# Kernel tuning notes

Hardware: AMD Instinct MI355X
Metric: run time of the kernel (lower is better)

The kernel has to match this reference:

```python
import jax, jax.numpy as jnp
import numpy as np

D_IN = 2048
D_OUT = 2048
NUM_HEADS = 16
NUM_GROUPS = 4
HEAD_DIM = D_OUT // NUM_HEADS          # 128
HEADS_PER_GROUP = NUM_HEADS // NUM_GROUPS  # 4


def setup_inputs() -> dict:
    key = jax.random.key(0)
    ks = jax.random.split(key, 6)
    b, s = 2, 2048
    x = jax.random.normal(ks[0], (b, s, D_IN), dtype=jnp.float32)
    # Store weights as [in, out] so y = x @ W (equivalent to torch Linear x @ W.T)
    sc_q = 1.0 / np.sqrt(D_IN)
    Wq = jax.random.uniform(ks[1], (D_IN, D_OUT), jnp.float32, -sc_q, sc_q)
    Wk = jax.random.uniform(ks[2], (D_IN, NUM_GROUPS * HEAD_DIM), jnp.float32, -sc_q, sc_q)
    Wv = jax.random.uniform(ks[3], (D_IN, NUM_GROUPS * HEAD_DIM), jnp.float32, -sc_q, sc_q)
    sc_o = 1.0 / np.sqrt(D_OUT)
    Wo = jax.random.uniform(ks[4], (D_OUT, D_OUT), jnp.float32, -sc_o, sc_o)
    bo = jax.random.uniform(ks[5], (D_OUT,), jnp.float32, -sc_o, sc_o)
    return {"x": x, "Wq": Wq, "Wk": Wk, "Wv": Wv, "Wo": Wo, "bo": bo}


def reference(x, Wq, Wk, Wv, Wo, bo):
    b, s, _ = x.shape
    g, hpg, hd = NUM_GROUPS, HEADS_PER_GROUP, HEAD_DIM
    # Projections; keep grouped layout instead of repeat_interleave (same math)
    q = (x @ Wq).reshape(b, s, g, hpg, hd)   # query heads ordered group-major,
                                             # matching repeat_interleave of K/V
    k = (x @ Wk).reshape(b, s, g, hd)
    v = (x @ Wv).reshape(b, s, g, hd)
    # scores: [b, g, hpg, q_len, k_len]
    scores = jnp.einsum('bqghd,bkgd->bghqk', q, k)
    causal = jnp.triu(jnp.ones((s, s), dtype=bool), k=1)  # True above diagonal
    scores = jnp.where(causal, -jnp.inf, scores)
    scale = 1.0 / jnp.sqrt(jnp.asarray(hd, dtype=scores.dtype))
    attn = jax.nn.softmax(scores * scale, axis=-1)
    ctx = jnp.einsum('bghqk,bkgd->bqghd', attn, v).reshape(b, s, D_OUT)
    return ctx @ Wo + bo
```

## Files before the change

### kernel.cpp

```cpp
#include <hip/hip_runtime.h>

typedef short v8s __attribute__((ext_vector_type(8)));
typedef float v4f __attribute__((ext_vector_type(4)));

__device__ __forceinline__ short f2bf(float f) {
  union { float f; unsigned u; } v; v.f = f;
  unsigned r = v.u + 0x7FFFu + ((v.u >> 16) & 1u);
  return (short)(r >> 16);
}

__device__ __forceinline__ void gll16(const short* g, short* l) {
  __builtin_amdgcn_global_load_lds(
      (const __attribute__((address_space(1))) void*)g,
      (__attribute__((address_space(3))) void*)l, 16, 0, 0);
}

__global__ void cast_f32_bf16(const float* __restrict__ in, short* __restrict__ out, int n4) {
  int i = blockIdx.x * blockDim.x + threadIdx.x;
  if (i >= n4) return;
  float4 v = ((const float4*)in)[i];
  short4 o;
  o.x = f2bf(v.x); o.y = f2bf(v.y); o.z = f2bf(v.z); o.w = f2bf(v.w);
  ((short4*)out)[i] = o;
}

__global__ void cast_transpose_weights(const float* __restrict__ Wq, const float* __restrict__ Wk,
                                       const float* __restrict__ Wv, const float* __restrict__ Wo,
                                       short* __restrict__ Wqkvt, short* __restrict__ Wot) {
  __shared__ float tile[32][33];
  const int tx = threadIdx.x, ty = threadIdx.y;
  int bx = blockIdx.x;
  const float* src; short* dst; int C, cb;
  if (bx < 64)      { src = Wq; dst = Wqkvt;                        C = 2048; cb = bx; }
  else if (bx < 80) { src = Wk; dst = Wqkvt + (size_t)2048 * 2048;  C = 512;  cb = bx - 64; }
  else if (bx < 96) { src = Wv; dst = Wqkvt + (size_t)2560 * 2048;  C = 512;  cb = bx - 80; }
  else              { src = Wo; dst = Wot;                          C = 2048; cb = bx - 96; }
  const int c0 = cb * 32, r0 = blockIdx.y * 32;
#pragma unroll
  for (int i = 0; i < 4; ++i)
    tile[ty + 8 * i][tx] = src[(size_t)(r0 + ty + 8 * i) * C + c0 + tx];
  __syncthreads();
#pragma unroll
  for (int i = 0; i < 4; ++i)
    dst[(size_t)(c0 + ty + 8 * i) * 2048 + r0 + tx] = f2bf(tile[tx][ty + 8 * i]);
}

__global__ void transpose_v_perm(const short* __restrict__ qkv, short* __restrict__ out) {
  __shared__ short tile[32][33];
  const int tx = threadIdx.x, ty = threadIdx.y;
  const int c0 = blockIdx.x * 32, r0 = blockIdx.y * 32;
  const int z = blockIdx.z;
#pragma unroll
  for (int i = 0; i < 4; ++i)
    tile[ty + 8 * i][tx] = qkv[(size_t)(z * 2048 + r0 + ty + 8 * i) * 3072 + 2560 + c0 + tx];
  __syncthreads();
#pragma unroll
  for (int i = 0; i < 4; ++i) {
    int k = r0 + tx;
    int pk = (k & ~31) | ((((k >> 2) & 3) * 2 + ((k >> 4) & 1)) * 4) | (k & 3);
    out[(size_t)z * 512 * 2048 + (size_t)(c0 + ty + 8 * i) * 2048 + pk] = tile[tx][ty + 8 * i];
  }
}

template <int BF16_OUT>
__global__ __launch_bounds__(256) void gemm_bt(const short* __restrict__ A,
                                               const short* __restrict__ Bt,
                                               void* __restrict__ Cout,
                                               const float* __restrict__ bias,
                                               int M, int N, int K) {
  __shared__ short As[128 * 32];
  __shared__ short Bs[128 * 32];
  const int tid = threadIdx.x;
  const int m0 = blockIdx.y * 128, n0 = blockIdx.x * 128;
  const int w = tid >> 6, lane = tid & 63, quad = lane >> 4, l16 = lane & 15;
  const int wm = (w >> 1) * 64, wn = (w & 1) * 64;
  v4f acc[4][4] = {};
  const int srow = lane >> 2, scol = (lane & 3) * 8;
  const short* Ap = A + (size_t)(m0 + w * 32 + srow) * K + scol;
  const short* Bp = Bt + (size_t)(n0 + w * 32 + srow) * K + scol;
  short* AsW = &As[(w * 32) * 32 + lane * 8];
  short* BsW = &Bs[(w * 32) * 32 + lane * 8];
  const size_t rstep = (size_t)16 * K;
  for (int k0 = 0; k0 < K; k0 += 32) {
    __syncthreads();
    gll16(Ap, AsW);
    gll16(Ap + rstep, AsW + 16 * 32);
    gll16(Bp, BsW);
    gll16(Bp + rstep, BsW + 16 * 32);
    __syncthreads();
    Ap += 32; Bp += 32;
    v8s af[4], bf[4];
#pragma unroll
    for (int i = 0; i < 4; ++i) af[i] = *(const v8s*)&As[(wm + i * 16 + l16) * 32 + quad * 8];
#pragma unroll
    for (int i = 0; i < 4; ++i) bf[i] = *(const v8s*)&Bs[(wn + i * 16 + l16) * 32 + quad * 8];
#pragma unroll
    for (int mi = 0; mi < 4; ++mi)
#pragma unroll
      for (int ni = 0; ni < 4; ++ni)
        acc[mi][ni] = __builtin_amdgcn_mfma_f32_16x16x32_bf16(af[mi], bf[ni], acc[mi][ni], 0, 0, 0);
  }
#pragma unroll
  for (int mi = 0; mi < 4; ++mi) {
#pragma unroll
    for (int ni = 0; ni < 4; ++ni) {
      const int col = n0 + wn + ni * 16 + l16;
#pragma unroll
      for (int r = 0; r < 4; ++r) {
        const int row = m0 + wm + mi * 16 + quad * 4 + r;
        if (BF16_OUT) {
          ((short*)Cout)[(size_t)row * N + col] = f2bf(acc[mi][ni][r]);
        } else {
          ((float*)Cout)[(size_t)row * N + col] = acc[mi][ni][r] + bias[col];
        }
      }
    }
  }
}

__global__ __launch_bounds__(256, 1) void flash_attn4(const short* __restrict__ QKV,
                                                      const short* __restrict__ Vtb,
                                                      short* __restrict__ ctx) {
  __shared__ __align__(16) short smem[32768];
  const int tid = threadIdx.x;
  const int w = tid >> 6, lane = tid & 63, quad = lane >> 4, l16 = lane & 15;
  const int wq = w >> 1, wk = w & 1;
  const int bh = blockIdx.y;
  const int b = bh >> 4, h = bh & 15, g = h >> 2;
  const float scale = 0.08838834764831845f;
  v8s ones;
#pragma unroll
  for (int i = 0; i < 8; ++i) ones[i] = (short)0x3F80;

  const int krl = lane >> 4, kcl = lane & 15;
  const int vrl = lane >> 3, vcl = lane & 7;
  const short* Kg0 = QKV + (size_t)(b * 2048 + w * 16 + krl) * 3072 + 2048 + g * 128;
  const short* Vg0 = Vtb + (size_t)(b * 512 + g * 128 + w * 32 + vrl) * 2048 + (vcl ^ (vrl & 7)) * 8;
  short* kd = smem + (w * 16) * 128 + lane * 8;
  short* vd = smem + 8192 + (w * 32) * 64 + lane * 8;

  auto stage = [&](int key0, int bs) {
    const short* kg = Kg0 + (size_t)key0 * 3072;
    const short* vg = Vg0 + key0;
#pragma unroll
    for (int ii = 0; ii < 4; ++ii) {
      const int rl = (ii * 4 + krl) & 15;
      gll16(kg + (size_t)(ii * 4) * 3072 + (kcl ^ rl) * 8, kd + bs * 16384 + ii * 512);
      gll16(vg + (size_t)(ii * 8) * 2048, vd + bs * 16384 + ii * 512);
    }
  };

  float* red = (float*)smem;

#pragma unroll 1
  for (int half = 0; half < 2; ++half) {
    const int qt = half ? (15 - blockIdx.x) : blockIdx.x;
    const int q0 = qt * 128;
    const int qb = q0 + wq * 64;

    v8s aq[4][4];
#pragma unroll
    for (int qs = 0; qs < 4; ++qs) {
      const short* Qp = QKV + (size_t)(b * 2048 + qb + qs * 16 + l16) * 3072 + h * 128 + quad * 8;
#pragma unroll
      for (int kk = 0; kk < 4; ++kk) aq[qs][kk] = *(const v8s*)(Qp + kk * 32);
    }
    v4f o[4][8] = {};
    v4f ol[4] = {};

    __syncthreads();
    stage(0, 0);
    const int nk = 2 * qt + 2;
#pragma unroll 1
    for (int kt = 0; kt < nk; ++kt) {
      const int key0 = kt << 6;
      __syncthreads();
      if (kt + 1 < nk) stage((kt + 1) << 6, (kt + 1) & 1);
      const short* Ks = smem + (kt & 1) * 16384;
      const short* Vs = Ks + 8192;
      const int kb = key0 + wk * 32;
      if (kb > qb + 63) continue;
      v4f sf[4][2] = {};
#pragma unroll
      for (int kfl = 0; kfl < 2; ++kfl)
#pragma unroll
        for (int kk = 0; kk < 4; ++kk) {
          v8s kfr = *(const v8s*)&Ks[((wk * 2 + kfl) * 16 + l16) * 128 + (((kk * 4 + quad) ^ l16) * 8)];
#pragma unroll
          for (int qs = 0; qs < 4; ++qs)
            sf[qs][kfl] = __builtin_amdgcn_mfma_f32_16x16x32_bf16(kfr, aq[qs][kk], sf[qs][kfl], 0, 0, 0);
        }
      const bool diag = (kb + 31 > qb);
      v8s pa[4];
#pragma unroll
      for (int qs = 0; qs < 4; ++qs) {
        const int qg = qb + qs * 16 + l16;
        v8s t;
#pragma unroll
        for (int kfl = 0; kfl < 2; ++kfl)
#pragma unroll
          for (int r = 0; r < 4; ++r) {
            float s = sf[qs][kfl][r] * scale;
            if (diag && (kb + kfl * 16 + quad * 4 + r > qg)) s = -1e30f;
            t[kfl * 4 + r] = f2bf(__expf(s));
          }
        pa[qs] = t;
      }
#pragma unroll
      for (int nf = 0; nf < 8; ++nf) {
        v8s vf = *(const v8s*)&Vs[(nf * 16 + l16) * 64 + (((wk * 4 + quad) ^ (l16 & 7)) * 8)];
#pragma unroll
        for (int qs = 0; qs < 4; ++qs)
          o[qs][nf] = __builtin_amdgcn_mfma_f32_16x16x32_bf16(pa[qs], vf, o[qs][nf], 0, 0, 0);
      }
#pragma unroll
      for (int qs = 0; qs < 4; ++qs)
        ol[qs] = __builtin_amdgcn_mfma_f32_16x16x32_bf16(pa[qs], ones, ol[qs], 0, 0, 0);
    }
    __syncthreads();

    if (wk == 1) {
#pragma unroll
      for (int qs = 0; qs < 4; ++qs)
        *(v4f*)&red[(wq * 4 + qs) * 256 + l16 * 16 + quad * 4] = ol[qs];
    }
    __syncthreads();
    if (wk == 0) {
#pragma unroll
      for (int qs = 0; qs < 4; ++qs)
        ol[qs] += *(const v4f*)&red[(wq * 4 + qs) * 256 + l16 * 16 + quad * 4];
    }
    __syncthreads();
    if (wk == 1) {
#pragma unroll
      for (int qs = 0; qs < 4; ++qs)
#pragma unroll
        for (int nf = 0; nf < 8; ++nf)
          *(v4f*)&red[(((wq * 4 + qs) * 8 + nf) * 256) + l16 * 16 + quad * 4] = o[qs][nf];
    }
    __syncthreads();
    if (wk == 0) {
#pragma unroll
      for (int qs = 0; qs < 4; ++qs) {
        float inv[4];
#pragma unroll
        for (int r = 0; r < 4; ++r) inv[r] = 1.0f / ol[qs][r];
#pragma unroll
        for (int nf = 0; nf < 8; ++nf) {
          v4f osum = o[qs][nf] + *(const v4f*)&red[(((wq * 4 + qs) * 8 + nf) * 256) + l16 * 16 + quad * 4];
#pragma unroll
          for (int r = 0; r < 4; ++r) {
            const int row = qb + qs * 16 + quad * 4 + r;
            ctx[(size_t)(b * 2048 + row) * 2048 + h * 128 + nf * 16 + l16] = f2bf(osum[r] * inv[r]);
          }
        }
      }
    }
  }
}

extern "C" void kernel_launch(void* const* d_in, const int* in_sizes, int n_in,
                              void* d_out, int out_size, void* d_ws, size_t ws_size,
                              hipStream_t stream) {
  const float* x = (const float*)d_in[0];
  const float* Wq = (const float*)d_in[1];
  const float* Wk = (const float*)d_in[2];
  const float* Wv = (const float*)d_in[3];
  const float* Wo = (const float*)d_in[4];
  const float* bo = (const float*)d_in[5];
  float* out = (float*)d_out;
  char* ws = (char*)d_ws;

  short* xb    = (short*)(ws);
  short* ctx   = (short*)(ws);
  short* Wqkvt = (short*)(ws + 16777216);
  short* Wot   = (short*)(ws + 29360128);
  short* QKV   = (short*)(ws + 37748736);
  short* Vtb   = (short*)(ws + 62914560);

  dim3 tb(32, 8);
  cast_f32_bf16<<<8192, 256, 0, stream>>>(x, xb, 2097152);
  cast_transpose_weights<<<dim3(160, 64), tb, 0, stream>>>(Wq, Wk, Wv, Wo, Wqkvt, Wot);

  gemm_bt<1><<<dim3(24, 32), 256, 0, stream>>>(xb, Wqkvt, (void*)QKV, nullptr, 4096, 3072, 2048);

  transpose_v_perm<<<dim3(16, 64, 2), tb, 0, stream>>>(QKV, Vtb);

  flash_attn4<<<dim3(8, 32), 256, 0, stream>>>(QKV, Vtb, ctx);

  gemm_bt<0><<<dim3(16, 32), 256, 0, stream>>>(ctx, Wot, (void*)out, bo, 4096, 2048, 2048);
}
```

Before: 335.0 us.

## Split attention keys across four waves and fold softmax scale into Q projection

The attention kernel moves to 512 threads with four key-split waves per query half, processing 128-key tiles from a single-buffered LDS stage instead of double-buffered 64-key tiles. The softmax scale and log2(e) are folded into the Q projection epilogue so the inner loop uses exp2f without a multiply. Partial sums from the four key waves are reduced through LDS in several sequential steps. The aim is more parallelism and fewer ALU ops per score, at the cost of losing load/compute overlap and adding reduction barriers.

```diff
diff --git a/kernel.cpp b/kernel.cpp
--- a/kernel.cpp
+++ b/kernel.cpp
@@ -62,12 +62,12 @@
   }
 }
 
-template <int BF16_OUT>
+template <int BF16_OUT, int SCALEQ>
 __global__ __launch_bounds__(256) void gemm_bt(const short* __restrict__ A,
                                                const short* __restrict__ Bt,
                                                void* __restrict__ Cout,
                                                const float* __restrict__ bias,
-                                               int M, int N, int K) {
+                                               int M, int N, int K, float qalpha) {
   __shared__ short As[128 * 32];
   __shared__ short Bs[128 * 32];
   const int tid = threadIdx.x;
@@ -105,11 +105,12 @@
 #pragma unroll
     for (int ni = 0; ni < 4; ++ni) {
       const int col = n0 + wn + ni * 16 + l16;
+      const float cs = (SCALEQ && col < 2048) ? qalpha : 1.0f;
 #pragma unroll
       for (int r = 0; r < 4; ++r) {
         const int row = m0 + wm + mi * 16 + quad * 4 + r;
         if (BF16_OUT) {
-          ((short*)Cout)[(size_t)row * N + col] = f2bf(acc[mi][ni][r]);
+          ((short*)Cout)[(size_t)row * N + col] = f2bf(acc[mi][ni][r] * cs);
         } else {
           ((float*)Cout)[(size_t)row * N + col] = acc[mi][ni][r] + bias[col];
         }
@@ -118,37 +119,27 @@
   }
 }
 
-__global__ __launch_bounds__(256, 1) void flash_attn4(const short* __restrict__ QKV,
+__global__ __launch_bounds__(512, 2) void flash_attn5(const short* __restrict__ QKV,
                                                       const short* __restrict__ Vtb,
                                                       short* __restrict__ ctx) {
   __shared__ __align__(16) short smem[32768];
+  short* Ks = smem;
+  short* Vs = smem + 16384;
   const int tid = threadIdx.x;
   const int w = tid >> 6, lane = tid & 63, quad = lane >> 4, l16 = lane & 15;
-  const int wq = w >> 1, wk = w & 1;
+  const int wq = w >> 2, wk = w & 3;
   const int bh = blockIdx.y;
   const int b = bh >> 4, h = bh & 15, g = h >> 2;
-  const float scale = 0.08838834764831845f;
   v8s ones;
 #pragma unroll
   for (int i = 0; i < 8; ++i) ones[i] = (short)0x3F80;
 
-  const int krl = lane >> 4, kcl = lane & 15;
-  const int vrl = lane >> 3, vcl = lane & 7;
-  const short* Kg0 = QKV + (size_t)(b * 2048 + w * 16 + krl) * 3072 + 2048 + g * 128;
-  const short* Vg0 = Vtb + (size_t)(b * 512 + g * 128 + w * 32 + vrl) * 2048 + (vcl ^ (vrl & 7)) * 8;
-  short* kd = smem + (w * 16) * 128 + lane * 8;
-  short* vd = smem + 8192 + (w * 32) * 64 + lane * 8;
-
-  auto stage = [&](int key0, int bs) {
-    const short* kg = Kg0 + (size_t)key0 * 3072;
-    const short* vg = Vg0 + key0;
-#pragma unroll
-    for (int ii = 0; ii < 4; ++ii) {
-      const int rl = (ii * 4 + krl) & 15;
-      gll16(kg + (size_t)(ii * 4) * 3072 + (kcl ^ rl) * 8, kd + bs * 16384 + ii * 512);
-      gll16(vg + (size_t)(ii * 8) * 2048, vd + bs * 16384 + ii * 512);
-    }
-  };
+  const int srow0 = w * 16 + (lane >> 4);
+  const int slot = lane & 15;
+  short* kdst = Ks + srow0 * 128 + slot * 8;
+  short* vdst = Vs + srow0 * 128 + slot * 8;
+  const short* Kg0 = QKV + (size_t)(b * 2048 + srow0) * 3072 + 2048 + g * 128;
+  const short* Vg0 = Vtb + (size_t)(b * 512 + g * 128 + srow0) * 2048;
 
   float* red = (float*)smem;
 
@@ -168,24 +159,30 @@
     v4f o[4][8] = {};
     v4f ol[4] = {};
 
-    __syncthreads();
-    stage(0, 0);
-    const int nk = 2 * qt + 2;
+    const int nk = qt + 1;
 #pragma unroll 1
     for (int kt = 0; kt < nk; ++kt) {
-      const int key0 = kt << 6;
+      const int key0 = kt << 7;
       __syncthreads();
-      if (kt + 1 < nk) stage((kt + 1) << 6, (kt + 1) & 1);
-      const short* Ks = smem + (kt & 1) * 16384;
-      const short* Vs = Ks + 8192;
+      {
+#pragma unroll
+        for (int ii = 0; ii < 4; ++ii) {
+          const int rlow = (lane >> 4) + ii * 4;
+          gll16(Kg0 + (size_t)(key0 + ii * 4) * 3072 + (slot ^ rlow) * 8, kdst + ii * 4 * 128);
+          gll16(Vg0 + (size_t)(ii * 4) * 2048 + key0 + (slot ^ rlow) * 8, vdst + ii * 4 * 128);
+        }
+      }
+      __syncthreads();
+
       const int kb = key0 + wk * 32;
       if (kb > qb + 63) continue;
+
       v4f sf[4][2] = {};
 #pragma unroll
       for (int kfl = 0; kfl < 2; ++kfl)
 #pragma unroll
         for (int kk = 0; kk < 4; ++kk) {
-          v8s kfr = *(const v8s*)&Ks[((wk * 2 + kfl) * 16 + l16) * 128 + (((kk * 4 + quad) ^ l16) * 8)];
+          v8s kfr = *(const v8s*)&Ks[(wk * 32 + kfl * 16 + l16) * 128 + (((kk * 4 + quad) ^ l16) * 8)];
 #pragma unroll
           for (int qs = 0; qs < 4; ++qs)
             sf[qs][kfl] = __builtin_amdgcn_mfma_f32_16x16x32_bf16(kfr, aq[qs][kk], sf[qs][kfl], 0, 0, 0);
@@ -200,15 +197,15 @@
         for (int kfl = 0; kfl < 2; ++kfl)
 #pragma unroll
           for (int r = 0; r < 4; ++r) {
-            float s = sf[qs][kfl][r] * scale;
+            float s = sf[qs][kfl][r];
             if (diag && (kb + kfl * 16 + quad * 4 + r > qg)) s = -1e30f;
-            t[kfl * 4 + r] = f2bf(__expf(s));
+            t[kfl * 4 + r] = f2bf(exp2f(s));
           }
         pa[qs] = t;
       }
 #pragma unroll
       for (int nf = 0; nf < 8; ++nf) {
-        v8s vf = *(const v8s*)&Vs[(nf * 16 + l16) * 64 + (((wk * 4 + quad) ^ (l16 & 7)) * 8)];
+        v8s vf = *(const v8s*)&Vs[(nf * 16 + l16) * 128 + (((wk * 4 + quad) ^ l16) * 8)];
 #pragma unroll
         for (int qs = 0; qs < 4; ++qs)
           o[qs][nf] = __builtin_amdgcn_mfma_f32_16x16x32_bf16(pa[qs], vf, o[qs][nf], 0, 0, 0);
@@ -217,44 +214,67 @@
       for (int qs = 0; qs < 4; ++qs)
         ol[qs] = __builtin_amdgcn_mfma_f32_16x16x32_bf16(pa[qs], ones, ol[qs], 0, 0, 0);
     }
-    __syncthreads();
-
+
+    __syncthreads();
+#pragma unroll
+    for (int qs = 0; qs < 4; ++qs)
+      *(v4f*)&red[(((wk * 2 + wq) * 4 + qs) * 256) + l16 * 16 + quad * 4] = ol[qs];
+    __syncthreads();
+    float inv[4][4];
+    if (wk == 0) {
+#pragma unroll
+      for (int qs = 0; qs < 4; ++qs) {
+        v4f lsum = ol[qs];
+#pragma unroll
+        for (int j = 1; j < 4; ++j)
+          lsum += *(const v4f*)&red[(((j * 2 + wq) * 4 + qs) * 256) + l16 * 16 + quad * 4];
+#pragma unroll
+        for (int r = 0; r < 4; ++r) inv[qs][r] = 1.0f / lsum[r];
+      }
+    }
+    __syncthreads();
+    if (wk == 3) {
+#pragma unroll
+      for (int qs = 0; qs < 4; ++qs)
+#pragma unroll
+        for (int nf = 0; nf < 8; ++nf)
+          *(v4f*)&red[((((wq * 4 + qs) * 8 + nf) * 256)) + l16 * 16 + quad * 4] = o[qs][nf];
+    }
+    __syncthreads();
+    if (wk == 2) {
+#pragma unroll
+      for (int qs = 0; qs < 4; ++qs)
+#pragma unroll
+        for (int nf = 0; nf < 8; ++nf) {
+          float* p = &red[((((wq * 4 + qs) * 8 + nf) * 256)) + l16 * 16 + quad * 4];
+          *(v4f*)p = o[qs][nf] + *(const v4f*)p;
+        }
+    }
+    __syncthreads();
     if (wk == 1) {
 #pragma unroll
       for (int qs = 0; qs < 4; ++qs)
-        *(v4f*)&red[(wq * 4 + qs) * 256 + l16 * 16 + quad * 4] = ol[qs];
+#pragma unroll
+        for (int nf = 0; nf < 8; ++nf) {
+          float* p = &red[((((wq * 4 + qs) * 8 + nf) * 256)) + l16 * 16 + quad * 4];
+          *(v4f*)p = o[qs][nf] + *(const v4f*)p;
+        }
     }
     __syncthreads();
     if (wk == 0) {
 #pragma unroll
       for (int qs = 0; qs < 4; ++qs)
-        ol[qs] += *(const v4f*)&red[(wq * 4 + qs) * 256 + l16 * 16 + quad * 4];
-    }
-    __syncthreads();
-    if (wk == 1) {
-#pragma unroll
-      for (int qs = 0; qs < 4; ++qs)
-#pragma unroll
-        for (int nf = 0; nf < 8; ++nf)
-          *(v4f*)&red[(((wq * 4 + qs) * 8 + nf) * 256) + l16 * 16 + quad * 4] = o[qs][nf];
-    }
-    __syncthreads();
-    if (wk == 0) {
-#pragma unroll
-      for (int qs = 0; qs < 4; ++qs) {
-        float inv[4];
-#pragma unroll
-        for (int r = 0; r < 4; ++r) inv[r] = 1.0f / ol[qs][r];
 #pragma unroll
         for (int nf = 0; nf < 8; ++nf) {
-          v4f osum = o[qs][nf] + *(const v4f*)&red[(((wq * 4 + qs) * 8 + nf) * 256) + l16 * 16 + quad * 4];
+          v4f osum = o[qs][nf] +
+                     *(const v4f*)&red[((((wq * 4 + qs) * 8 + nf) * 256)) + l16 * 16 + quad * 4];
 #pragma unroll
           for (int r = 0; r < 4; ++r) {
             const int row = qb + qs * 16 + quad * 4 + r;
-            ctx[(size_t)(b * 2048 + row) * 2048 + h * 128 + nf * 16 + l16] = f2bf(osum[r] * inv[r]);
+            ctx[(size_t)(b * 2048 + row) * 2048 + h * 128 + nf * 16 + l16] =
+                f2bf(osum[r] * inv[qs][r]);
           }
         }
-      }
     }
   }
 }
@@ -278,15 +298,17 @@
   short* QKV   = (short*)(ws + 37748736);
   short* Vtb   = (short*)(ws + 62914560);
 
+  const float qalpha = 0.08838834764831845f * 1.4426950408889634f;
+
   dim3 tb(32, 8);
   cast_f32_bf16<<<8192, 256, 0, stream>>>(x, xb, 2097152);
   cast_transpose_weights<<<dim3(160, 64), tb, 0, stream>>>(Wq, Wk, Wv, Wo, Wqkvt, Wot);
 
-  gemm_bt<1><<<dim3(24, 32), 256, 0, stream>>>(xb, Wqkvt, (void*)QKV, nullptr, 4096, 3072, 2048);
+  gemm_bt<1, 1><<<dim3(24, 32), 256, 0, stream>>>(xb, Wqkvt, (void*)QKV, nullptr, 4096, 3072, 2048, qalpha);
 
   transpose_v_perm<<<dim3(16, 64, 2), tb, 0, stream>>>(QKV, Vtb);
 
-  flash_attn4<<<dim3(8, 32), 256, 0, stream>>>(QKV, Vtb, ctx);
-
-  gemm_bt<0><<<dim3(16, 32), 256, 0, stream>>>(ctx, Wot, (void*)out, bo, 4096, 2048, 2048);
-}
+  flash_attn5<<<dim3(8, 32), 512, 0, stream>>>(QKV, Vtb, ctx);
+
+  gemm_bt<0, 0><<<dim3(16, 32), 256, 0, stream>>>(ctx, Wot, (void*)out, bo, 4096, 2048, 2048, 1.0f);
+}
```

Result: slower. 438.0 us (+30.7%).
